# Optimization experiments

Measured on AMD Instinct MI355X. Metric: run time of the kernel, lower is better.

## Reference

```python
import jax, jax.numpy as jnp
import numpy as np

N_QUBITS = 4
LAYERS = 2
NUM_HEADS = 8
EMBED = 32
DK = EMBED // NUM_HEADS  # == N_QUBITS
B, S = 32, 4096


def _ry(t):
    c, s = jnp.cos(t / 2), jnp.sin(t / 2)
    m = jnp.stack([jnp.stack([c, -s], -1), jnp.stack([s, c], -1)], -2)
    return m.astype(jnp.complex64)


def _rx(t):
    c = jnp.cos(t / 2).astype(jnp.complex64)
    s = (-1j) * jnp.sin(t / 2).astype(jnp.complex64)
    return jnp.stack([jnp.stack([c, s], -1), jnp.stack([s, c], -1)], -2)


def _rz(t):
    em = jnp.exp(-0.5j * t.astype(jnp.complex64))
    ep = jnp.conj(em)
    z = jnp.zeros_like(em)
    return jnp.stack([jnp.stack([em, z], -1), jnp.stack([z, ep], -1)], -2)


def _apply_1q(state, U, w, n):
    # state: (B, 2**n); wire 0 is the most-significant bit (PennyLane convention)
    s = state.reshape(-1, 2 ** w, 2, 2 ** (n - 1 - w))
    if U.ndim == 2:  # shared gate
        s = jnp.einsum('ij,bpjq->bpiq', U, s)
    else:  # per-token gate, U: (B,2,2)
        s = jnp.einsum('bij,bpjq->bpiq', U, s)
    return s.reshape(-1, 2 ** n)


def _cnot(state, c, t, n):
    s = state.reshape((-1,) + (2,) * n)
    c_ax, t_ax = 1 + c, 1 + t
    s0 = jax.lax.slice_in_dim(s, 0, 1, axis=c_ax)
    s1 = jax.lax.slice_in_dim(s, 1, 2, axis=c_ax)
    s1 = jnp.flip(s1, axis=t_ax)  # X on target where control == 1
    s = jnp.concatenate([s0, s1], axis=c_ax)
    return s.reshape(-1, 2 ** n)


def _z_expvals(state, n):
    p = jnp.abs(state) ** 2  # (B, 2**n)
    outs = []
    for i in range(n):
        pr = p.reshape(-1, 2 ** i, 2, 2 ** (n - 1 - i))
        outs.append(pr[:, :, 0, :].sum((1, 2)) - pr[:, :, 1, :].sum((1, 2)))
    return jnp.stack(outs, -1)  # (B, n)


def _head_fwd(x_h, p_h):
    # x_h: (BT, n_qubits) angles, p_h: (layers, n_qubits, 3)
    n, L = N_QUBITS, LAYERS
    bt = x_h.shape[0]
    state = jnp.zeros((bt, 2 ** n), jnp.complex64).at[:, 0].set(1.0)
    for i in range(n):
        state = _apply_1q(state, _ry(x_h[:, i]), i, n)
    for l in range(L):
        for i in range(n):
            state = _apply_1q(state, _rx(p_h[l, i, 0]), i, n)
            state = _apply_1q(state, _ry(p_h[l, i, 1]), i, n)
            state = _apply_1q(state, _rz(p_h[l, i, 2]), i, n)
        for i in range(n - 1):
            state = _cnot(state, i, i + 1, n)
        state = _cnot(state, n - 1, 0, n)
    return _z_expvals(state, n)


def setup_inputs() -> dict:
    key = jax.random.key(0)
    k1, k2, k3, k4 = jax.random.split(key, 4)
    x = jax.random.normal(k1, (B, S, EMBED), jnp.float32)
    params = jax.random.normal(k2, (NUM_HEADS, LAYERS, N_QUBITS, 3), jnp.float32)
    fan_in = NUM_HEADS * N_QUBITS
    bound = 1.0 / np.sqrt(fan_in)
    W_out = jax.random.uniform(k3, (EMBED, fan_in), jnp.float32, -bound, bound)
    b_out = jax.random.uniform(k4, (EMBED,), jnp.float32, -bound, bound)
    return {'x': x, 'params': params, 'W_out': W_out, 'b_out': b_out}


def reference(x, params, W_out, b_out):
    b, s, e = x.shape
    xh = x.reshape(b, s, NUM_HEADS, DK)
    xh = jnp.moveaxis(xh, 2, 0).reshape(NUM_HEADS, b * s, DK)  # (H, BT, d_k)
    ang = xh[:, :, :N_QUBITS]  # angles fed into RY embedding
    ev = jax.vmap(_head_fwd)(ang, params)  # (H, BT, n_qubits)
    concat = jnp.moveaxis(ev, 0, 1).reshape(b, s, NUM_HEADS * N_QUBITS)
    return concat @ W_out.T + b_out
```

## Files before the change

kernel.cpp:

```cpp
#include <hip/hip_runtime.h>
#include <math.h>

#define NQ   4
#define NH   8
#define NL   2
#define DIM  16
#define EMB  32
#define TPB  256

#define LO_SCALE 4096.0f
#define LO_INV   (1.0f/4096.0f)

typedef _Float16 f16x8  __attribute__((ext_vector_type(8)));
typedef float    f32x16 __attribute__((ext_vector_type(16)));

__global__ void build_unitaries_kernel(const float* __restrict__ params,
                                       const float* __restrict__ W,
                                       float* __restrict__ Uws) {
    int tid = threadIdx.x;
    int h   = tid >> 4;
    int col = tid & 15;

    float re[DIM], im[DIM];
#pragma unroll
    for (int j = 0; j < DIM; ++j) { re[j] = (j == col) ? 1.f : 0.f; im[j] = 0.f; }

#pragma unroll
    for (int l = 0; l < NL; ++l) {
#pragma unroll
        for (int q = 0; q < NQ; ++q) {
            const float* p = params + ((h * NL + l) * NQ + q) * 3;
            const int m = 1 << (3 - q);
            {
                float s, c; __sincosf(0.5f * p[0], &s, &c);
#pragma unroll
                for (int j = 0; j < DIM; ++j) {
                    if (j & m) continue;
                    const int j1 = j | m;
                    float r0 = re[j], i0 = im[j], r1 = re[j1], i1 = im[j1];
                    re[j]  = c * r0 + s * i1;
                    im[j]  = c * i0 - s * r1;
                    re[j1] = s * i0 + c * r1;
                    im[j1] = -s * r0 + c * i1;
                }
            }
            {
                float s, c; __sincosf(0.5f * p[1], &s, &c);
#pragma unroll
                for (int j = 0; j < DIM; ++j) {
                    if (j & m) continue;
                    const int j1 = j | m;
                    float r0 = re[j], i0 = im[j], r1 = re[j1], i1 = im[j1];
                    re[j]  = c * r0 - s * r1;
                    im[j]  = c * i0 - s * i1;
                    re[j1] = s * r0 + c * r1;
                    im[j1] = s * i0 + c * i1;
                }
            }
            {
                float s, c; __sincosf(0.5f * p[2], &s, &c);
#pragma unroll
                for (int j = 0; j < DIM; ++j) {
                    if (j & m) continue;
                    const int j1 = j | m;
                    float r0 = re[j], i0 = im[j], r1 = re[j1], i1 = im[j1];
                    re[j]  = c * r0 + s * i0;
                    im[j]  = c * i0 - s * r0;
                    re[j1] = c * r1 - s * i1;
                    im[j1] = c * i1 + s * r1;
                }
            }
        }
#pragma unroll
        for (int e = 0; e < NQ; ++e) {
            const int cm = 1 << (3 - e), tm = 1 << (3 - ((e + 1) & 3));
#pragma unroll
            for (int j = 0; j < DIM; ++j) {
                if ((j & cm) && !(j & tm)) {
                    const int j1 = j | tm;
                    float tr = re[j]; re[j] = re[j1]; re[j1] = tr;
                    float ti = im[j]; im[j] = im[j1]; im[j1] = ti;
                }
            }
        }
    }

    _Float16* Ah = (_Float16*)Uws;
    _Float16* Al = Ah + 4096;
    const int khigh = col >> 3, e = col & 7;
#pragma unroll
    for (int j = 0; j < DIM; ++j) {
        {
            const float v = re[j];
            const _Float16 h16 = (_Float16)v;
            const float lo = (v - (float)h16) * LO_SCALE;
            const int lane = j + 32 * khigh;
            Ah[(h * 64 + lane) * 8 + e] = h16;
            Al[(h * 64 + lane) * 8 + e] = (_Float16)lo;
        }
        {
            const float v = im[j];
            const _Float16 h16 = (_Float16)v;
            const float lo = (v - (float)h16) * LO_SCALE;
            const int lane = 16 + j + 32 * khigh;
            Ah[(h * 64 + lane) * 8 + e] = h16;
            Al[(h * 64 + lane) * 8 + e] = (_Float16)lo;
        }
    }

    if (tid < 64) {
        const int eo = tid & 31, kh = tid >> 5;
        _Float16* Wf = ((_Float16*)Uws) + 8192 + tid * 32;
#pragma unroll
        for (int j = 0; j < 8; ++j) {
            const float v0 = W[eo * EMB + kh * 8 + j];
            const float v1 = W[eo * EMB + 16 + kh * 8 + j];
            const _Float16 h0 = (_Float16)v0;
            const _Float16 h1 = (_Float16)v1;
            Wf[j]      = h0;
            Wf[8 + j]  = h1;
            Wf[16 + j] = (_Float16)((v0 - (float)h0) * LO_SCALE);
            Wf[24 + j] = (_Float16)((v1 - (float)h1) * LO_SCALE);
        }
    }
}

__global__ __launch_bounds__(512, 4)
void qmha_kernel(const float* __restrict__ x,
                 const float* __restrict__ Uws,
                 const float* __restrict__ bvec,
                 float* __restrict__ out,
                 int ntok) {
    __shared__ float evs[EMB * TPB];

    const int tid  = threadIdx.x;
    const int tok0 = blockIdx.x * TPB;
    const int lane = tid & 63;
    const int lh   = lane & 31;
    const int hi   = lane >> 5;

    f32x16 zz;
#pragma unroll
    for (int i = 0; i < 16; ++i) zz[i] = 0.f;

    {
        const int h = __builtin_amdgcn_readfirstlane(tid >> 6);

        const _Float16* Ahp = (const _Float16*)Uws;
        const _Float16* Alp = Ahp + 4096;
        const f16x8 Afh = *(const f16x8*)(Ahp + (h * 64 + lane) * 8);
        const f16x8 Afl = *(const f16x8*)(Alp + (h * 64 + lane) * 8);

#pragma unroll 2
        for (int g = 0; g < 8; ++g) {
            const int t    = g * 32 + lh;
            const int tok  = tok0 + t;
            const int tokc = (tok < ntok) ? tok : (ntok - 1);

            const float4 xa = *(const float4*)(x + (size_t)tokc * EMB + h * NQ);
            float c0, s0, c1, s1, c2, s2, c3, s3;
            __sincosf(0.5f * xa.x, &s0, &c0);
            __sincosf(0.5f * xa.y, &s1, &c1);
            __sincosf(0.5f * xa.z, &s2, &c2);
            __sincosf(0.5f * xa.w, &s3, &c3);

            const float f  = hi ? s0 : c0;
            const float pA = f * c1, pB = f * s1;
            const float p23[4] = {c2 * c3, c2 * s3, s2 * c3, s2 * s3};

            f16x8 bh, bl;
#pragma unroll
            for (int e = 0; e < 8; ++e) {
                const float av = ((e >> 2) ? pB : pA) * p23[e & 3];
                const _Float16 ah16 = (_Float16)av;
                bh[e] = ah16;
                bl[e] = (_Float16)((av - (float)ah16) * LO_SCALE);
            }

            f32x16 accH = __builtin_amdgcn_mfma_f32_32x32x16_f16(Afh, bh, zz, 0, 0, 0);
            f32x16 accL = __builtin_amdgcn_mfma_f32_32x32x16_f16(Afl, bh, zz, 0, 0, 0);
            accL = __builtin_amdgcn_mfma_f32_32x32x16_f16(Afh, bl, accL, 0, 0, 0);

            float pj[8];
#pragma unroll
            for (int r = 0; r < 8; ++r) {
                const float ar = fmaf(accL[r],     LO_INV, accH[r]);
                const float ai = fmaf(accL[r + 8], LO_INV, accH[r + 8]);
                pj[r] = ar * ar + ai * ai;
            }
            const float s01 = pj[0] + pj[1], s23 = pj[2] + pj[3];
            const float s45 = pj[4] + pj[5], s67 = pj[6] + pj[7];
            const float sa = s01 + s23, sb = s45 + s67;
            float ev0 = sa - sb;
            const float tot = sa + sb;
            float ev1 = hi ? -tot : tot;
            float ev2 = (s01 + s45) - (s23 + s67);
            float ev3 = (pj[0] - pj[1]) + (pj[2] - pj[3]) +
                        (pj[4] - pj[5]) + (pj[6] - pj[7]);
            ev0 += __shfl_xor(ev0, 32);
            ev1 += __shfl_xor(ev1, 32);
            ev2 += __shfl_xor(ev2, 32);
            ev3 += __shfl_xor(ev3, 32);

            if (hi == 0 && tok < ntok) {
                evs[(h * 4 + 0) * TPB + t] = ev0;
                evs[(h * 4 + 1) * TPB + t] = ev1;
                evs[(h * 4 + 2) * TPB + t] = ev2;
                evs[(h * 4 + 3) * TPB + t] = ev3;
            }
        }
    }
    __syncthreads();

    {
        const int w = tid >> 6;
        const _Float16* Wf = ((const _Float16*)Uws) + 8192 + lane * 32;
        const f16x8 Wh0 = *(const f16x8*)(Wf + 0);
        const f16x8 Wh1 = *(const f16x8*)(Wf + 8);
        const f16x8 Wl0 = *(const f16x8*)(Wf + 16);
        const f16x8 Wl1 = *(const f16x8*)(Wf + 24);
        const float bias = bvec[lh];

        const float* evp = evs + w * 32 + lh;
        f16x8 Ah0, Ah1, Al0, Al1;
#pragma unroll
        for (int e = 0; e < 8; ++e) {
            const int k0 = hi * 8 + e;
            const float v0 = evp[k0 * TPB];
            const float v1 = evp[(16 + k0) * TPB];
            const _Float16 a0 = (_Float16)v0;
            const _Float16 a1 = (_Float16)v1;
            Ah0[e] = a0;
            Ah1[e] = a1;
            Al0[e] = (_Float16)((v0 - (float)a0) * LO_SCALE);
            Al1[e] = (_Float16)((v1 - (float)a1) * LO_SCALE);
        }

        f32x16 aH = __builtin_amdgcn_mfma_f32_32x32x16_f16(Ah0, Wh0, zz, 0, 0, 0);
        aH = __builtin_amdgcn_mfma_f32_32x32x16_f16(Ah1, Wh1, aH, 0, 0, 0);
        f32x16 aL = __builtin_amdgcn_mfma_f32_32x32x16_f16(Al0, Wh0, zz, 0, 0, 0);
        aL = __builtin_amdgcn_mfma_f32_32x32x16_f16(Al1, Wh1, aL, 0, 0, 0);
        aL = __builtin_amdgcn_mfma_f32_32x32x16_f16(Ah0, Wl0, aL, 0, 0, 0);
        aL = __builtin_amdgcn_mfma_f32_32x32x16_f16(Ah1, Wl1, aL, 0, 0, 0);

#pragma unroll
        for (int r = 0; r < 16; ++r) {
            const int trow = (r & 3) + 8 * (r >> 2) + 4 * hi;
            const int tok  = tok0 + w * 32 + trow;
            if (tok < ntok) {
                out[(size_t)tok * EMB + lh] =
                    fmaf(aL[r], LO_INV, aH[r]) + bias;
            }
        }
    }
}

extern "C" void kernel_launch(void* const* d_in, const int* in_sizes, int n_in,
                              void* d_out, int out_size, void* d_ws, size_t ws_size,
                              hipStream_t stream) {
    const float* x      = (const float*)d_in[0];
    const float* params = (const float*)d_in[1];
    const float* W_out  = (const float*)d_in[2];
    const float* b_out  = (const float*)d_in[3];
    float*       out    = (float*)d_out;
    float*       Uws    = (float*)d_ws;

    const int ntok = in_sizes[0] / EMB;

    hipLaunchKernelGGL(build_unitaries_kernel, dim3(1), dim3(128), 0, stream,
                       params, W_out, Uws);

    const int blocks = (ntok + TPB - 1) / TPB;
    hipLaunchKernelGGL(qmha_kernel, dim3(blocks), dim3(512), 0, stream,
                       x, Uws, b_out, out, ntok);
}
```

Before: 88.09 us.

## Fuse unitary construction into main kernel and prefetch next token group

Removes the separate single-block build_unitaries launch: every block now rebuilds the 8 per-head 16x16 unitaries in LDS using its first 128 threads, then syncs before the MFMA loop. The W matrix is split into high/low fp16 parts in registers instead of being read from workspace. It also software-prefetches the next group's x float4 before the current group's compute. This trades one kernel launch and a serialised tiny kernel for redundant per-block unitary work, which takes register-heavy serial time at the start of each of the 512 blocks and uses extra LDS.

After: 87.50 us. No clear change (-0.7%).

```diff
diff --git a/kernel.cpp b/kernel.cpp
--- a/kernel.cpp
+++ b/kernel.cpp
@@ -10,159 +10,149 @@
 
 #define LO_SCALE 4096.0f
 #define LO_INV   (1.0f/4096.0f)
+#define HSTR 520
 
 typedef _Float16 f16x8  __attribute__((ext_vector_type(8)));
 typedef float    f32x16 __attribute__((ext_vector_type(16)));
 
-__global__ void build_unitaries_kernel(const float* __restrict__ params,
-                                       const float* __restrict__ W,
-                                       float* __restrict__ Uws) {
-    int tid = threadIdx.x;
-    int h   = tid >> 4;
-    int col = tid & 15;
-
-    float re[DIM], im[DIM];
-#pragma unroll
-    for (int j = 0; j < DIM; ++j) { re[j] = (j == col) ? 1.f : 0.f; im[j] = 0.f; }
-
-#pragma unroll
-    for (int l = 0; l < NL; ++l) {
-#pragma unroll
-        for (int q = 0; q < NQ; ++q) {
-            const float* p = params + ((h * NL + l) * NQ + q) * 3;
-            const int m = 1 << (3 - q);
-            {
-                float s, c; __sincosf(0.5f * p[0], &s, &c);
-#pragma unroll
-                for (int j = 0; j < DIM; ++j) {
-                    if (j & m) continue;
-                    const int j1 = j | m;
-                    float r0 = re[j], i0 = im[j], r1 = re[j1], i1 = im[j1];
-                    re[j]  = c * r0 + s * i1;
-                    im[j]  = c * i0 - s * r1;
-                    re[j1] = s * i0 + c * r1;
-                    im[j1] = -s * r0 + c * i1;
-                }
-            }
-            {
-                float s, c; __sincosf(0.5f * p[1], &s, &c);
-#pragma unroll
-                for (int j = 0; j < DIM; ++j) {
-                    if (j & m) continue;
-                    const int j1 = j | m;
-                    float r0 = re[j], i0 = im[j], r1 = re[j1], i1 = im[j1];
-                    re[j]  = c * r0 - s * r1;
-                    im[j]  = c * i0 - s * i1;
-                    re[j1] = s * r0 + c * r1;
-                    im[j1] = s * i0 + c * i1;
-                }
-            }
-            {
-                float s, c; __sincosf(0.5f * p[2], &s, &c);
-#pragma unroll
-                for (int j = 0; j < DIM; ++j) {
-                    if (j & m) continue;
-                    const int j1 = j | m;
-                    float r0 = re[j], i0 = im[j], r1 = re[j1], i1 = im[j1];
-                    re[j]  = c * r0 + s * i0;
-                    im[j]  = c * i0 - s * r0;
-                    re[j1] = c * r1 - s * i1;
-                    im[j1] = c * i1 + s * r1;
-                }
-            }
-        }
-#pragma unroll
-        for (int e = 0; e < NQ; ++e) {
-            const int cm = 1 << (3 - e), tm = 1 << (3 - ((e + 1) & 3));
-#pragma unroll
-            for (int j = 0; j < DIM; ++j) {
-                if ((j & cm) && !(j & tm)) {
-                    const int j1 = j | tm;
-                    float tr = re[j]; re[j] = re[j1]; re[j1] = tr;
-                    float ti = im[j]; im[j] = im[j1]; im[j1] = ti;
-                }
-            }
-        }
-    }
-
-    _Float16* Ah = (_Float16*)Uws;
-    _Float16* Al = Ah + 4096;
-    const int khigh = col >> 3, e = col & 7;
-#pragma unroll
-    for (int j = 0; j < DIM; ++j) {
-        {
-            const float v = re[j];
-            const _Float16 h16 = (_Float16)v;
-            const float lo = (v - (float)h16) * LO_SCALE;
-            const int lane = j + 32 * khigh;
-            Ah[(h * 64 + lane) * 8 + e] = h16;
-            Al[(h * 64 + lane) * 8 + e] = (_Float16)lo;
-        }
-        {
-            const float v = im[j];
-            const _Float16 h16 = (_Float16)v;
-            const float lo = (v - (float)h16) * LO_SCALE;
-            const int lane = 16 + j + 32 * khigh;
-            Ah[(h * 64 + lane) * 8 + e] = h16;
-            Al[(h * 64 + lane) * 8 + e] = (_Float16)lo;
-        }
-    }
-
-    if (tid < 64) {
-        const int eo = tid & 31, kh = tid >> 5;
-        _Float16* Wf = ((_Float16*)Uws) + 8192 + tid * 32;
-#pragma unroll
-        for (int j = 0; j < 8; ++j) {
-            const float v0 = W[eo * EMB + kh * 8 + j];
-            const float v1 = W[eo * EMB + 16 + kh * 8 + j];
-            const _Float16 h0 = (_Float16)v0;
-            const _Float16 h1 = (_Float16)v1;
-            Wf[j]      = h0;
-            Wf[8 + j]  = h1;
-            Wf[16 + j] = (_Float16)((v0 - (float)h0) * LO_SCALE);
-            Wf[24 + j] = (_Float16)((v1 - (float)h1) * LO_SCALE);
-        }
-    }
-}
-
 __global__ __launch_bounds__(512, 4)
-void qmha_kernel(const float* __restrict__ x,
-                 const float* __restrict__ Uws,
-                 const float* __restrict__ bvec,
-                 float* __restrict__ out,
-                 int ntok) {
-    __shared__ float evs[EMB * TPB];
+void qmha_fused(const float* __restrict__ x,
+                const float* __restrict__ params,
+                const float* __restrict__ W,
+                const float* __restrict__ bvec,
+                float* __restrict__ out,
+                int ntok) {
+    __shared__ _Float16 AfH[NH * HSTR];
+    __shared__ _Float16 AfL[NH * HSTR];
+    __shared__ float    evs[EMB * TPB];
 
     const int tid  = threadIdx.x;
     const int tok0 = blockIdx.x * TPB;
     const int lane = tid & 63;
     const int lh   = lane & 31;
     const int hi   = lane >> 5;
+    const int wv   = tid >> 6;
 
     f32x16 zz;
 #pragma unroll
     for (int i = 0; i < 16; ++i) zz[i] = 0.f;
 
+    float4 xa_cur;
     {
-        const int h = __builtin_amdgcn_readfirstlane(tid >> 6);
-
-        const _Float16* Ahp = (const _Float16*)Uws;
-        const _Float16* Alp = Ahp + 4096;
-        const f16x8 Afh = *(const f16x8*)(Ahp + (h * 64 + lane) * 8);
-        const f16x8 Afl = *(const f16x8*)(Alp + (h * 64 + lane) * 8);
+        int tk = tok0 + lh; if (tk >= ntok) tk = ntok - 1;
+        xa_cur = *(const float4*)(x + (size_t)tk * EMB + wv * NQ);
+    }
+
+    if (tid < 128) {
+        const int h   = tid >> 4;
+        const int col = tid & 15;
+
+        float re[DIM], im[DIM];
+#pragma unroll
+        for (int j = 0; j < DIM; ++j) { re[j] = (j == col) ? 1.f : 0.f; im[j] = 0.f; }
+
+#pragma unroll
+        for (int l = 0; l < NL; ++l) {
+#pragma unroll
+            for (int q = 0; q < NQ; ++q) {
+                const float* p = params + ((h * NL + l) * NQ + q) * 3;
+                const int m = 1 << (3 - q);
+                {
+                    float s, c; __sincosf(0.5f * p[0], &s, &c);
+#pragma unroll
+                    for (int j = 0; j < DIM; ++j) {
+                        if (j & m) continue;
+                        const int j1 = j | m;
+                        float r0 = re[j], i0 = im[j], r1 = re[j1], i1 = im[j1];
+                        re[j]  = c * r0 + s * i1;
+                        im[j]  = c * i0 - s * r1;
+                        re[j1] = s * i0 + c * r1;
+                        im[j1] = -s * r0 + c * i1;
+                    }
+                }
+                {
+                    float s, c; __sincosf(0.5f * p[1], &s, &c);
+#pragma unroll
+                    for (int j = 0; j < DIM; ++j) {
+                        if (j & m) continue;
+                        const int j1 = j | m;
+                        float r0 = re[j], i0 = im[j], r1 = re[j1], i1 = im[j1];
+                        re[j]  = c * r0 - s * r1;
+                        im[j]  = c * i0 - s * i1;
+                        re[j1] = s * r0 + c * r1;
+                        im[j1] = s * i0 + c * i1;
+                    }
+                }
+                {
+                    float s, c; __sincosf(0.5f * p[2], &s, &c);
+#pragma unroll
+                    for (int j = 0; j < DIM; ++j) {
+                        if (j & m) continue;
+                        const int j1 = j | m;
+                        float r0 = re[j], i0 = im[j], r1 = re[j1], i1 = im[j1];
+                        re[j]  = c * r0 + s * i0;
+                        im[j]  = c * i0 - s * r0;
+                        re[j1] = c * r1 - s * i1;
+                        im[j1] = c * i1 + s * r1;
+                    }
+                }
+            }
+#pragma unroll
+            for (int e = 0; e < NQ; ++e) {
+                const int cm = 1 << (3 - e), tm = 1 << (3 - ((e + 1) & 3));
+#pragma unroll
+                for (int j = 0; j < DIM; ++j) {
+                    if ((j & cm) && !(j & tm)) {
+                        const int j1 = j | tm;
+                        float tr = re[j]; re[j] = re[j1]; re[j1] = tr;
+                        float ti = im[j]; im[j] = im[j1]; im[j1] = ti;
+                    }
+                }
+            }
+        }
+
+        const int khigh = col >> 3, e = col & 7;
+#pragma unroll
+        for (int j = 0; j < DIM; ++j) {
+            {
+                const float v = re[j];
+                const _Float16 h16 = (_Float16)v;
+                const int ln = j + 32 * khigh;
+                AfH[h * HSTR + ln * 8 + e] = h16;
+                AfL[h * HSTR + ln * 8 + e] = (_Float16)((v - (float)h16) * LO_SCALE);
+            }
+            {
+                const float v = im[j];
+                const _Float16 h16 = (_Float16)v;
+                const int ln = 16 + j + 32 * khigh;
+                AfH[h * HSTR + ln * 8 + e] = h16;
+                AfL[h * HSTR + ln * 8 + e] = (_Float16)((v - (float)h16) * LO_SCALE);
+            }
+        }
+    }
+    __syncthreads();
+
+    {
+        const int h = wv;
+        const f16x8 Afh = *(const f16x8*)(AfH + h * HSTR + lane * 8);
+        const f16x8 Afl = *(const f16x8*)(AfL + h * HSTR + lane * 8);
 
 #pragma unroll 2
         for (int g = 0; g < 8; ++g) {
-            const int t    = g * 32 + lh;
-            const int tok  = tok0 + t;
-            const int tokc = (tok < ntok) ? tok : (ntok - 1);
-
-            const float4 xa = *(const float4*)(x + (size_t)tokc * EMB + h * NQ);
+            float4 xa_next = xa_cur;
+            if (g < 7) {
+                int tk = tok0 + (g + 1) * 32 + lh; if (tk >= ntok) tk = ntok - 1;
+                xa_next = *(const float4*)(x + (size_t)tk * EMB + h * NQ);
+            }
+
+            const int t   = g * 32 + lh;
+            const int tok = tok0 + t;
+
             float c0, s0, c1, s1, c2, s2, c3, s3;
-            __sincosf(0.5f * xa.x, &s0, &c0);
-            __sincosf(0.5f * xa.y, &s1, &c1);
-            __sincosf(0.5f * xa.z, &s2, &c2);
-            __sincosf(0.5f * xa.w, &s3, &c3);
+            __sincosf(0.5f * xa_cur.x, &s0, &c0);
+            __sincosf(0.5f * xa_cur.y, &s1, &c1);
+            __sincosf(0.5f * xa_cur.z, &s2, &c2);
+            __sincosf(0.5f * xa_cur.w, &s3, &c3);
 
             const float f  = hi ? s0 : c0;
             const float pA = f * c1, pB = f * s1;
@@ -208,17 +198,33 @@
                 evs[(h * 4 + 2) * TPB + t] = ev2;
                 evs[(h * 4 + 3) * TPB + t] = ev3;
             }
+            xa_cur = xa_next;
         }
     }
     __syncthreads();
 
     {
-        const int w = tid >> 6;
-        const _Float16* Wf = ((const _Float16*)Uws) + 8192 + lane * 32;
-        const f16x8 Wh0 = *(const f16x8*)(Wf + 0);
-        const f16x8 Wh1 = *(const f16x8*)(Wf + 8);
-        const f16x8 Wl0 = *(const f16x8*)(Wf + 16);
-        const f16x8 Wl1 = *(const f16x8*)(Wf + 24);
+        const int w = wv;
+        const float* wp = W + lh * EMB + hi * 8;
+        float wa[8], wb[8];
+        {
+            const float4 a0 = *(const float4*)(wp + 0);
+            const float4 a1 = *(const float4*)(wp + 4);
+            const float4 b0 = *(const float4*)(wp + 16);
+            const float4 b1 = *(const float4*)(wp + 20);
+            wa[0]=a0.x; wa[1]=a0.y; wa[2]=a0.z; wa[3]=a0.w;
+            wa[4]=a1.x; wa[5]=a1.y; wa[6]=a1.z; wa[7]=a1.w;
+            wb[0]=b0.x; wb[1]=b0.y; wb[2]=b0.z; wb[3]=b0.w;
+            wb[4]=b1.x; wb[5]=b1.y; wb[6]=b1.z; wb[7]=b1.w;
+        }
+        f16x8 Wh0, Wl0, Wh1, Wl1;
+#pragma unroll
+        for (int e = 0; e < 8; ++e) {
+            _Float16 hh = (_Float16)wa[e];
+            Wh0[e] = hh; Wl0[e] = (_Float16)((wa[e] - (float)hh) * LO_SCALE);
+            hh = (_Float16)wb[e];
+            Wh1[e] = hh; Wl1[e] = (_Float16)((wb[e] - (float)hh) * LO_SCALE);
+        }
         const float bias = bvec[lh];
 
         const float* evp = evs + w * 32 + lh;
@@ -263,14 +269,11 @@
     const float* W_out  = (const float*)d_in[2];
     const float* b_out  = (const float*)d_in[3];
     float*       out    = (float*)d_out;
-    float*       Uws    = (float*)d_ws;
+    (void)d_ws; (void)ws_size;
 
     const int ntok = in_sizes[0] / EMB;
 
-    hipLaunchKernelGGL(build_unitaries_kernel, dim3(1), dim3(128), 0, stream,
-                       params, W_out, Uws);
-
     const int blocks = (ntok + TPB - 1) / TPB;
-    hipLaunchKernelGGL(qmha_kernel, dim3(blocks), dim3(512), 0, stream,
-                       x, Uws, b_out, out, ntok);
+    hipLaunchKernelGGL(qmha_fused, dim3(blocks), dim3(512), 0, stream,
+                       x, params, W_out, b_out, out, ntok);
 }
```
